# Kernel tuning notes

Hardware: AMD Instinct MI355X
Metric: run time of the kernel (lower is better)

The kernel has to match this reference:

```python
import jax, jax.numpy as jnp
import numpy as np

D_MODEL = 1024
NUM_HEADS = 16
DEPTH = D_MODEL // NUM_HEADS


def setup_inputs() -> dict:
    key = jax.random.key(0)
    ks = jax.random.split(key, 5)
    B, S = 2, 2048
    scale = 1.0 / np.sqrt(D_MODEL)
    x = jax.random.normal(ks[0], (B, S, D_MODEL), dtype=jnp.float32)
    wq = jax.random.normal(ks[1], (D_MODEL, D_MODEL), dtype=jnp.float32) * scale
    wk = jax.random.normal(ks[2], (D_MODEL, D_MODEL), dtype=jnp.float32) * scale
    wv = jax.random.normal(ks[3], (D_MODEL, D_MODEL), dtype=jnp.float32) * scale
    wo = jax.random.normal(ks[4], (D_MODEL, D_MODEL), dtype=jnp.float32) * scale
    zb = jnp.zeros((D_MODEL,), dtype=jnp.float32)
    return {"x": x, "wq": wq, "bq": zb, "wk": wk, "bk": zb, "wv": wv, "bv": zb, "wo": wo, "bo": zb}


def _split_heads(t):
    # [B, S, D] -> [B, H, S, depth]
    B, S, _ = t.shape
    return t.reshape(B, S, NUM_HEADS, DEPTH).transpose(0, 2, 1, 3)


def reference(x, wq, bq, wk, bk, wv, bv, wo, bo):
    q = _split_heads(x @ wq + bq)
    k = _split_heads(x @ wk + bk)
    v = _split_heads(x @ wv + bv)
    scores = jnp.einsum("bhqd,bhkd->bhqk", q, k) / jnp.sqrt(jnp.float32(DEPTH))
    attn = jax.nn.softmax(scores, axis=-1)
    out = jnp.einsum("bhqk,bhkd->bhqd", attn, v)  # [B, H, S, depth]
    B, H, S, d = out.shape
    out = out.transpose(0, 2, 1, 3).reshape(B, S, D_MODEL)
    return out @ wo + bo
```

## Files before the change

### kernel.cpp

```cpp
#include <hip/hip_runtime.h>
#include <stdint.h>

#define SS 2048
#define DM 1024
#define HD 16
#define DP 64
#define BB 2

#define QSCALE 0.18033688011112042f

typedef unsigned short u16;
typedef short bf16x8 __attribute__((ext_vector_type(8)));
typedef float f32x4 __attribute__((ext_vector_type(4)));

#if __has_builtin(__builtin_amdgcn_exp2f)
#define EXP2F __builtin_amdgcn_exp2f
#else
#define EXP2F exp2f
#endif

__device__ __forceinline__ u16 f2b(float f) {
  unsigned u = __builtin_bit_cast(unsigned, f);
  u = (u + 0x7fffu + ((u >> 16) & 1u)) >> 16;
  return (u16)u;
}

__device__ __forceinline__ void gl_lds16(const void* g, void* l) {
  __builtin_amdgcn_global_load_lds(
      (const __attribute__((address_space(1))) unsigned int*)g,
      (__attribute__((address_space(3))) unsigned int*)l, 16, 0, 0);
}

__global__ __launch_bounds__(256) void cast_bf16_kernel(const float* __restrict__ in,
                                                        u16* __restrict__ out, int n) {
  int i = (blockIdx.x * 256 + threadIdx.x) * 4;
  if (i + 3 < n) {
    float4 f = *reinterpret_cast<const float4*>(in + i);
    ushort4 o;
    o.x = f2b(f.x); o.y = f2b(f.y); o.z = f2b(f.z); o.w = f2b(f.w);
    *reinterpret_cast<ushort4*>(out + i) = o;
  }
}

__global__ __launch_bounds__(256) void tcast4_kernel(
    const float* __restrict__ w0, const float* __restrict__ w1,
    const float* __restrict__ w2, const float* __restrict__ w3,
    u16* __restrict__ o0, u16* __restrict__ o1, u16* __restrict__ o2, u16* __restrict__ o3) {
  __shared__ float tile[32][33];
  const int z = blockIdx.z;
  const float* in = z == 0 ? w0 : (z == 1 ? w1 : (z == 2 ? w2 : w3));
  u16* out = z == 0 ? o0 : (z == 1 ? o1 : (z == 2 ? o2 : o3));
  const float scale = z == 0 ? QSCALE : 1.f;
  int tx = threadIdx.x & 31, ty = threadIdx.x >> 5;
  int c0 = blockIdx.x * 32;
  int r0 = blockIdx.y * 32;
#pragma unroll
  for (int j = 0; j < 4; ++j)
    tile[ty + j * 8][tx] = in[(size_t)(r0 + ty + j * 8) * DM + c0 + tx];
  __syncthreads();
#pragma unroll
  for (int j = 0; j < 4; ++j)
    out[(size_t)(c0 + ty + j * 8) * DM + r0 + tx] = f2b(tile[tx][ty + j * 8] * scale);
}

__global__ __launch_bounds__(256) void gemm_qkv(
    const u16* __restrict__ A, const u16* __restrict__ BT,
    const float* __restrict__ b0, const float* __restrict__ b1, const float* __restrict__ b2,
    u16* __restrict__ Oq, u16* __restrict__ Ok, u16* __restrict__ Ovt, int M, int K) {
  __shared__ __align__(16) u16 As[128][32];
  __shared__ __align__(16) u16 Bs[128][32];
  const int t = threadIdx.x;
  const int w = t >> 6, l = t & 63;
  const int lr = l & 15, lg = l >> 4;
  const int wr = w >> 1, wc = w & 1;
  const int m0 = blockIdx.y * 128, n0 = blockIdx.x * 128;

  const u16* Ab = A + (size_t)m0 * K;
  const u16* Bb = BT + (size_t)n0 * K;
  const int arow = t >> 2, achk = (t & 3) * 8;

  f32x4 acc[4][4];
#pragma unroll
  for (int mi = 0; mi < 4; ++mi)
#pragma unroll
    for (int ni = 0; ni < 4; ++ni)
      acc[mi][ni] = (f32x4){0.f, 0.f, 0.f, 0.f};

  char* AsB = (char*)(&As[0][0]);
  char* BsB = (char*)(&Bs[0][0]);

  for (int k0 = 0; k0 < K; k0 += 32) {
    gl_lds16(Ab + (size_t)arow * K + k0 + achk, AsB + t * 16);
    gl_lds16(Ab + (size_t)(arow + 64) * K + k0 + achk, AsB + t * 16 + 4096);
    gl_lds16(Bb + (size_t)arow * K + k0 + achk, BsB + t * 16);
    gl_lds16(Bb + (size_t)(arow + 64) * K + k0 + achk, BsB + t * 16 + 4096);
    __syncthreads();
    bf16x8 af[4], bfr[4];
#pragma unroll
    for (int mi = 0; mi < 4; ++mi)
      af[mi] = *(const bf16x8*)&As[wr * 64 + mi * 16 + lr][lg * 8];
#pragma unroll
    for (int ni = 0; ni < 4; ++ni)
      bfr[ni] = *(const bf16x8*)&Bs[wc * 64 + ni * 16 + lr][lg * 8];
#pragma unroll
    for (int mi = 0; mi < 4; ++mi)
#pragma unroll
      for (int ni = 0; ni < 4; ++ni)
        acc[mi][ni] =
            __builtin_amdgcn_mfma_f32_16x16x32_bf16(af[mi], bfr[ni], acc[mi][ni], 0, 0, 0);
    __syncthreads();
  }

  const int proj = n0 >> 10;
  const float* bias = proj == 0 ? b0 : (proj == 1 ? b1 : b2);
  const float bsc = proj == 0 ? QSCALE : 1.f;
  const int nloc0 = n0 & 1023;
  if (proj == 2) {
#pragma unroll
    for (int mi = 0; mi < 4; ++mi)
#pragma unroll
      for (int ni = 0; ni < 4; ++ni) {
        int gm0 = m0 + wr * 64 + mi * 16 + lg * 4;
        int gn = nloc0 + wc * 64 + ni * 16 + lr;
        int s0 = gm0 & (SS - 1), b = gm0 >> 11;
        int h = gn >> 6, d = gn & 63;
        float bv = bias[gn];
        ushort4 pk;
        pk.x = f2b(acc[mi][ni][0] + bv);
        pk.y = f2b(acc[mi][ni][1] + bv);
        pk.z = f2b(acc[mi][ni][2] + bv);
        pk.w = f2b(acc[mi][ni][3] + bv);
        *reinterpret_cast<ushort4*>(Ovt + (((size_t)(b * HD + h)) * DP + d) * SS + s0) = pk;
      }
  } else {
    u16* Op = proj == 0 ? Oq : Ok;
#pragma unroll
    for (int mi = 0; mi < 4; ++mi)
#pragma unroll
      for (int ni = 0; ni < 4; ++ni)
#pragma unroll
        for (int i = 0; i < 4; ++i) {
          int gm = m0 + wr * 64 + mi * 16 + lg * 4 + i;
          int gn = nloc0 + wc * 64 + ni * 16 + lr;
          float vv = acc[mi][ni][i] + bias[gn] * bsc;
          int s = gm & (SS - 1), b = gm >> 11;
          int h = gn >> 6, d = gn & 63;
          Op[(((size_t)(b * HD + h)) * SS + s) * DP + d] = f2b(vv);
        }
  }
}

__global__ __launch_bounds__(256) void gemm_out(
    const u16* __restrict__ A, const u16* __restrict__ BT, const float* __restrict__ b0,
    float* __restrict__ FO, int M, int K) {
  __shared__ __align__(16) u16 As[128][64];
  __shared__ __align__(16) u16 Bs[64][64];
  const int t = threadIdx.x;
  const int w = t >> 6, l = t & 63;
  const int lr = l & 15, lg = l >> 4;
  const int m0 = blockIdx.y * 128, n0 = blockIdx.x * 64;

  const u16* Ab = A + (size_t)m0 * K;
  const u16* Bb = BT + (size_t)n0 * K;
  const int srow = t >> 3;
  const int schk = ((t & 7) ^ (srow & 7)) * 8;

  f32x4 acc[2][4];
#pragma unroll
  for (int mi = 0; mi < 2; ++mi)
#pragma unroll
    for (int ni = 0; ni < 4; ++ni)
      acc[mi][ni] = (f32x4){0.f, 0.f, 0.f, 0.f};

  char* AsB = (char*)(&As[0][0]);
  char* BsB = (char*)(&Bs[0][0]);

  for (int k0 = 0; k0 < K; k0 += 64) {
#pragma unroll
    for (int j = 0; j < 4; ++j)
      gl_lds16(Ab + (size_t)(srow + 32 * j) * K + k0 + schk, AsB + t * 16 + j * 4096);
#pragma unroll
    for (int j = 0; j < 2; ++j)
      gl_lds16(Bb + (size_t)(srow + 32 * j) * K + k0 + schk, BsB + t * 16 + j * 4096);
    __syncthreads();
    bf16x8 af[2][2], bfr[4][2];
#pragma unroll
    for (int mi = 0; mi < 2; ++mi) {
      int r = w * 32 + mi * 16 + lr;
#pragma unroll
      for (int kk = 0; kk < 2; ++kk)
        af[mi][kk] = *(const bf16x8*)&As[r][(((kk * 4 + lg) ^ (r & 7)) * 8)];
    }
#pragma unroll
    for (int ni = 0; ni < 4; ++ni) {
      int r = ni * 16 + lr;
#pragma unroll
      for (int kk = 0; kk < 2; ++kk)
        bfr[ni][kk] = *(const bf16x8*)&Bs[r][(((kk * 4 + lg) ^ (r & 7)) * 8)];
    }
#pragma unroll
    for (int mi = 0; mi < 2; ++mi)
#pragma unroll
      for (int ni = 0; ni < 4; ++ni)
#pragma unroll
        for (int kk = 0; kk < 2; ++kk)
          acc[mi][ni] =
              __builtin_amdgcn_mfma_f32_16x16x32_bf16(af[mi][kk], bfr[ni][kk], acc[mi][ni], 0, 0, 0);
    __syncthreads();
  }

#pragma unroll
  for (int mi = 0; mi < 2; ++mi)
#pragma unroll
    for (int ni = 0; ni < 4; ++ni)
#pragma unroll
      for (int i = 0; i < 4; ++i) {
        int gm = m0 + w * 32 + mi * 16 + lg * 4 + i;
        int gn = n0 + ni * 16 + lr;
        FO[(size_t)gm * DM + gn] = acc[mi][ni][i] + b0[gn];
      }
}

__global__ __launch_bounds__(512) void attn_kernel(const u16* __restrict__ Q,
                                                   const u16* __restrict__ K,
                                                   const u16* __restrict__ VT,
                                                   u16* __restrict__ O) {
  __shared__ __align__(16) u16 Ks[2][64 * 64];
  __shared__ __align__(16) u16 Vs[2][64 * 64];
  __shared__ __align__(16) u16 Ps[8][16][68];
  const int t = threadIdx.x, w = t >> 6, l = t & 63;
  const int lr = l & 15, lg = l >> 4;
  const int bh = blockIdx.y;
  const int q0 = blockIdx.x * 128;
  const u16* Qb = Q + (size_t)bh * SS * DP;
  const u16* Kb = K + (size_t)bh * SS * DP;
  const u16* Vb = VT + (size_t)bh * DP * SS;

  const int qrow = q0 + w * 16 + lr;
  bf16x8 qf[2];
  qf[0] = *(const bf16x8*)(Qb + (size_t)qrow * DP + lg * 8);
  qf[1] = *(const bf16x8*)(Qb + (size_t)qrow * DP + 32 + lg * 8);

  bf16x8 ones8;
#pragma unroll
  for (int j = 0; j < 8; ++j) ones8[j] = (short)0x3f80;

  f32x4 oacc[4];
  f32x4 lac = (f32x4){0.f, 0.f, 0.f, 0.f};
#pragma unroll
  for (int i = 0; i < 4; ++i) oacc[i] = (f32x4){0.f, 0.f, 0.f, 0.f};

  const int srow = t >> 3;
  const int schk = ((t & 7) ^ (srow & 7)) * 8;

  gl_lds16(Kb + (size_t)srow * DP + schk, (char*)Ks[0] + t * 16);
  gl_lds16(Vb + (size_t)srow * SS + 0 + schk, (char*)Vs[0] + t * 16);
  asm volatile("s_waitcnt vmcnt(0)" ::: "memory");
  __syncthreads();

  int cur = 0;
  for (int t0 = 0; t0 < SS; t0 += 64, cur ^= 1) {
    if (t0 + 64 < SS) {
      gl_lds16(Kb + (size_t)(t0 + 64 + srow) * DP + schk, (char*)Ks[cur ^ 1] + t * 16);
      gl_lds16(Vb + (size_t)srow * SS + (t0 + 64) + schk, (char*)Vs[cur ^ 1] + t * 16);
    }
    const u16* Kc = Ks[cur];
    const u16* Vc = Vs[cur];

    f32x4 sc[4];
#pragma unroll
    for (int n = 0; n < 4; ++n) sc[n] = (f32x4){0.f, 0.f, 0.f, 0.f};
#pragma unroll
    for (int n = 0; n < 4; ++n) {
      int r = n * 16 + lr;
#pragma unroll
      for (int kk = 0; kk < 2; ++kk) {
        int chk = ((kk * 4 + lg) ^ (r & 7)) * 8;
        bf16x8 bk8 = *(const bf16x8*)(Kc + r * 64 + chk);
        sc[n] = __builtin_amdgcn_mfma_f32_16x16x32_bf16(qf[kk], bk8, sc[n], 0, 0, 0);
      }
    }

#pragma unroll
    for (int n = 0; n < 4; ++n)
#pragma unroll
      for (int i = 0; i < 4; ++i)
        Ps[w][lg * 4 + i][n * 16 + lr] = f2b(EXP2F(sc[n][i]));
    asm volatile("s_waitcnt lgkmcnt(0)" ::: "memory");
    bf16x8 pf[2];
    pf[0] = *(const bf16x8*)&Ps[w][lr][lg * 8];
    pf[1] = *(const bf16x8*)&Ps[w][lr][32 + lg * 8];

#pragma unroll
    for (int kk = 0; kk < 2; ++kk)
      lac = __builtin_amdgcn_mfma_f32_16x16x32_bf16(pf[kk], ones8, lac, 0, 0, 0);

#pragma unroll
    for (int n = 0; n < 4; ++n) {
      int r = n * 16 + lr;
#pragma unroll
      for (int kk = 0; kk < 2; ++kk) {
        int chk = ((kk * 4 + lg) ^ (r & 7)) * 8;
        bf16x8 bv8 = *(const bf16x8*)(Vc + r * 64 + chk);
        oacc[n] = __builtin_amdgcn_mfma_f32_16x16x32_bf16(pf[kk], bv8, oacc[n], 0, 0, 0);
      }
    }
    asm volatile("s_waitcnt vmcnt(0)" ::: "memory");
    __syncthreads();
  }

  const int b = bh >> 4, h = bh & 15;
  float inv[4];
#pragma unroll
  for (int i = 0; i < 4; ++i) inv[i] = 1.0f / lac[i];
#pragma unroll
  for (int n = 0; n < 4; ++n)
#pragma unroll
    for (int i = 0; i < 4; ++i) {
      int row = q0 + w * 16 + lg * 4 + i;
      int col = h * 64 + n * 16 + lr;
      O[((size_t)(b * SS + row)) * DM + col] = f2b(oacc[n][i] * inv[i]);
    }
}

extern "C" void kernel_launch(void* const* d_in, const int* in_sizes, int n_in,
                              void* d_out, int out_size, void* d_ws, size_t ws_size,
                              hipStream_t stream) {
  const float* x = (const float*)d_in[0];
  const float* wq = (const float*)d_in[1];
  const float* bq = (const float*)d_in[2];
  const float* wk = (const float*)d_in[3];
  const float* bk = (const float*)d_in[4];
  const float* wv = (const float*)d_in[5];
  const float* bv = (const float*)d_in[6];
  const float* wo = (const float*)d_in[7];
  const float* bo = (const float*)d_in[8];
  float* out = (float*)d_out;

  u16* ws = (u16*)d_ws;
  u16* xb = ws;
  u16* wt3 = ws + 4194304;
  u16* wot = ws + 7340032;
  u16* q = ws + 8388608;
  u16* k = ws + 12582912;
  u16* vt = ws + 16777216;
  u16* o = ws;

  cast_bf16_kernel<<<4096, 256, 0, stream>>>(x, xb, 4194304);
  tcast4_kernel<<<dim3(32, 32, 4), 256, 0, stream>>>(wq, wk, wv, wo, wt3, wt3 + 1048576,
                                                     wt3 + 2097152, wot);

  gemm_qkv<<<dim3(24, 32), 256, 0, stream>>>(xb, wt3, bq, bk, bv, q, k, vt, 4096, 1024);
  attn_kernel<<<dim3(16, 32), 512, 0, stream>>>(q, k, vt, o);
  gemm_out<<<dim3(16, 32), 256, 0, stream>>>(o, wot, bo, out, 4096, 1024);
}
```

Before: 215.2 us.

## Keep attention probabilities in registers via transposed MFMA, widen QKV GEMM K-tile

The attention kernel now computes S^T = K·Q^T, so the exp'd scores already sit in the MFMA B-operand layout. They are packed with v_cvt_pk_bf16_f32 and fed straight into the PV and row-sum MFMAs, which removes the per-tile LDS round trip through Ps. K rows are loaded in a permuted order so that this register layout lines up with V. The kernel also moves to 256-thread blocks of 64 queries with an XCD-aware block-to-head remap, so blocks that share K/V data land on the same die. Separately, the QKV GEMM K-step goes from 32 to 64 with an XOR-swizzled LDS layout, halving the barriers per K; the cost is more LDS per block and harder-to-check index permutations.

New measurement: 197.8 us. 1.09x faster.

```diff
diff --git a/kernel.cpp b/kernel.cpp
--- a/kernel.cpp
+++ b/kernel.cpp
@@ -10,8 +10,10 @@
 #define QSCALE 0.18033688011112042f
 
 typedef unsigned short u16;
+typedef unsigned int u32;
 typedef short bf16x8 __attribute__((ext_vector_type(8)));
 typedef float f32x4 __attribute__((ext_vector_type(4)));
+typedef u32 u32x4 __attribute__((ext_vector_type(4)));
 
 #if __has_builtin(__builtin_amdgcn_exp2f)
 #define EXP2F __builtin_amdgcn_exp2f
@@ -23,6 +25,12 @@
   unsigned u = __builtin_bit_cast(unsigned, f);
   u = (u + 0x7fffu + ((u >> 16) & 1u)) >> 16;
   return (u16)u;
+}
+
+__device__ __forceinline__ u32 pk2(float a, float b) {
+  u32 r;
+  asm("v_cvt_pk_bf16_f32 %0, %1, %2" : "=v"(r) : "v"(a), "v"(b));
+  return r;
 }
 
 __device__ __forceinline__ void gl_lds16(const void* g, void* l) {
@@ -67,8 +75,8 @@
     const u16* __restrict__ A, const u16* __restrict__ BT,
     const float* __restrict__ b0, const float* __restrict__ b1, const float* __restrict__ b2,
     u16* __restrict__ Oq, u16* __restrict__ Ok, u16* __restrict__ Ovt, int M, int K) {
-  __shared__ __align__(16) u16 As[128][32];
-  __shared__ __align__(16) u16 Bs[128][32];
+  __shared__ __align__(16) u16 As[128][64];
+  __shared__ __align__(16) u16 Bs[128][64];
   const int t = threadIdx.x;
   const int w = t >> 6, l = t & 63;
   const int lr = l & 15, lg = l >> 4;
@@ -77,7 +85,8 @@
 
   const u16* Ab = A + (size_t)m0 * K;
   const u16* Bb = BT + (size_t)n0 * K;
-  const int arow = t >> 2, achk = (t & 3) * 8;
+  const int srow = t >> 3;
+  const int schk = ((t & 7) ^ (srow & 7)) * 8;
 
   f32x4 acc[4][4];
 #pragma unroll
@@ -89,25 +98,31 @@
   char* AsB = (char*)(&As[0][0]);
   char* BsB = (char*)(&Bs[0][0]);
 
-  for (int k0 = 0; k0 < K; k0 += 32) {
-    gl_lds16(Ab + (size_t)arow * K + k0 + achk, AsB + t * 16);
-    gl_lds16(Ab + (size_t)(arow + 64) * K + k0 + achk, AsB + t * 16 + 4096);
-    gl_lds16(Bb + (size_t)arow * K + k0 + achk, BsB + t * 16);
-    gl_lds16(Bb + (size_t)(arow + 64) * K + k0 + achk, BsB + t * 16 + 4096);
-    __syncthreads();
-    bf16x8 af[4], bfr[4];
-#pragma unroll
-    for (int mi = 0; mi < 4; ++mi)
-      af[mi] = *(const bf16x8*)&As[wr * 64 + mi * 16 + lr][lg * 8];
-#pragma unroll
-    for (int ni = 0; ni < 4; ++ni)
-      bfr[ni] = *(const bf16x8*)&Bs[wc * 64 + ni * 16 + lr][lg * 8];
-#pragma unroll
-    for (int mi = 0; mi < 4; ++mi)
+  for (int k0 = 0; k0 < K; k0 += 64) {
+#pragma unroll
+    for (int j = 0; j < 4; ++j)
+      gl_lds16(Ab + (size_t)(srow + 32 * j) * K + k0 + schk, AsB + t * 16 + j * 4096);
+#pragma unroll
+    for (int j = 0; j < 4; ++j)
+      gl_lds16(Bb + (size_t)(srow + 32 * j) * K + k0 + schk, BsB + t * 16 + j * 4096);
+    __syncthreads();
+#pragma unroll
+    for (int kk = 0; kk < 2; ++kk) {
+      bf16x8 af[4], bfr[4];
+      const int chk = ((kk * 4 + lg) ^ (lr & 7)) * 8;
+#pragma unroll
+      for (int mi = 0; mi < 4; ++mi)
+        af[mi] = *(const bf16x8*)&As[wr * 64 + mi * 16 + lr][chk];
 #pragma unroll
       for (int ni = 0; ni < 4; ++ni)
-        acc[mi][ni] =
-            __builtin_amdgcn_mfma_f32_16x16x32_bf16(af[mi], bfr[ni], acc[mi][ni], 0, 0, 0);
+        bfr[ni] = *(const bf16x8*)&Bs[wc * 64 + ni * 16 + lr][chk];
+#pragma unroll
+      for (int mi = 0; mi < 4; ++mi)
+#pragma unroll
+        for (int ni = 0; ni < 4; ++ni)
+          acc[mi][ni] =
+              __builtin_amdgcn_mfma_f32_16x16x32_bf16(af[mi], bfr[ni], acc[mi][ni], 0, 0, 0);
+    }
     __syncthreads();
   }
 
@@ -221,17 +236,20 @@
       }
 }
 
-__global__ __launch_bounds__(512) void attn_kernel(const u16* __restrict__ Q,
+__global__ __launch_bounds__(256) void attn_kernel(const u16* __restrict__ Q,
                                                    const u16* __restrict__ K,
                                                    const u16* __restrict__ VT,
                                                    u16* __restrict__ O) {
   __shared__ __align__(16) u16 Ks[2][64 * 64];
   __shared__ __align__(16) u16 Vs[2][64 * 64];
-  __shared__ __align__(16) u16 Ps[8][16][68];
   const int t = threadIdx.x, w = t >> 6, l = t & 63;
   const int lr = l & 15, lg = l >> 4;
-  const int bh = blockIdx.y;
-  const int q0 = blockIdx.x * 128;
+
+  const int wg = blockIdx.y * 32 + blockIdx.x;
+  const int xcd = wg & 7, idx = wg >> 3;
+  const int bh = xcd * 4 + (idx >> 5);
+  const int q0 = (idx & 31) * 64;
+
   const u16* Qb = Q + (size_t)bh * SS * DP;
   const u16* Kb = K + (size_t)bh * SS * DP;
   const u16* Vb = VT + (size_t)bh * DP * SS;
@@ -252,75 +270,76 @@
 
   const int srow = t >> 3;
   const int schk = ((t & 7) ^ (srow & 7)) * 8;
-
-  gl_lds16(Kb + (size_t)srow * DP + schk, (char*)Ks[0] + t * 16);
-  gl_lds16(Vb + (size_t)srow * SS + 0 + schk, (char*)Vs[0] + t * 16);
-  asm volatile("s_waitcnt vmcnt(0)" ::: "memory");
+  const int krow = (srow & 3) | ((srow & 12) << 1) | ((srow & 16) >> 2);
+  const int swz = (lr & 7);
+
+  gl_lds16(Kb + (size_t)krow * DP + schk, (char*)Ks[0] + t * 16);
+  gl_lds16(Kb + (size_t)(krow + 32) * DP + schk, (char*)Ks[0] + 4096 + t * 16);
+  gl_lds16(Vb + (size_t)srow * SS + schk, (char*)Vs[0] + t * 16);
+  gl_lds16(Vb + (size_t)(srow + 32) * SS + schk, (char*)Vs[0] + 4096 + t * 16);
   __syncthreads();
 
   int cur = 0;
   for (int t0 = 0; t0 < SS; t0 += 64, cur ^= 1) {
     if (t0 + 64 < SS) {
-      gl_lds16(Kb + (size_t)(t0 + 64 + srow) * DP + schk, (char*)Ks[cur ^ 1] + t * 16);
+      const u16* Kn = Kb + (size_t)(t0 + 64) * DP;
+      gl_lds16(Kn + (size_t)krow * DP + schk, (char*)Ks[cur ^ 1] + t * 16);
+      gl_lds16(Kn + (size_t)(krow + 32) * DP + schk, (char*)Ks[cur ^ 1] + 4096 + t * 16);
       gl_lds16(Vb + (size_t)srow * SS + (t0 + 64) + schk, (char*)Vs[cur ^ 1] + t * 16);
+      gl_lds16(Vb + (size_t)(srow + 32) * SS + (t0 + 64) + schk, (char*)Vs[cur ^ 1] + 4096 + t * 16);
     }
     const u16* Kc = Ks[cur];
     const u16* Vc = Vs[cur];
 
-    f32x4 sc[4];
-#pragma unroll
-    for (int n = 0; n < 4; ++n) sc[n] = (f32x4){0.f, 0.f, 0.f, 0.f};
-#pragma unroll
-    for (int n = 0; n < 4; ++n) {
-      int r = n * 16 + lr;
+    f32x4 st[4];
+#pragma unroll
+    for (int n = 0; n < 4; ++n) st[n] = (f32x4){0.f, 0.f, 0.f, 0.f};
+#pragma unroll
+    for (int n = 0; n < 4; ++n)
 #pragma unroll
       for (int kk = 0; kk < 2; ++kk) {
-        int chk = ((kk * 4 + lg) ^ (r & 7)) * 8;
-        bf16x8 bk8 = *(const bf16x8*)(Kc + r * 64 + chk);
-        sc[n] = __builtin_amdgcn_mfma_f32_16x16x32_bf16(qf[kk], bk8, sc[n], 0, 0, 0);
+        bf16x8 kf = *(const bf16x8*)(Kc + (n * 16 + lr) * 64 + (((kk * 4 + lg) ^ swz) * 8));
+        st[n] = __builtin_amdgcn_mfma_f32_16x16x32_bf16(kf, qf[kk], st[n], 0, 0, 0);
       }
-    }
-
+
+    float e[4][4];
 #pragma unroll
     for (int n = 0; n < 4; ++n)
 #pragma unroll
-      for (int i = 0; i < 4; ++i)
-        Ps[w][lg * 4 + i][n * 16 + lr] = f2b(EXP2F(sc[n][i]));
-    asm volatile("s_waitcnt lgkmcnt(0)" ::: "memory");
-    bf16x8 pf[2];
-    pf[0] = *(const bf16x8*)&Ps[w][lr][lg * 8];
-    pf[1] = *(const bf16x8*)&Ps[w][lr][32 + lg * 8];
-
-#pragma unroll
-    for (int kk = 0; kk < 2; ++kk)
-      lac = __builtin_amdgcn_mfma_f32_16x16x32_bf16(pf[kk], ones8, lac, 0, 0, 0);
-
-#pragma unroll
-    for (int n = 0; n < 4; ++n) {
-      int r = n * 16 + lr;
-#pragma unroll
-      for (int kk = 0; kk < 2; ++kk) {
-        int chk = ((kk * 4 + lg) ^ (r & 7)) * 8;
-        bf16x8 bv8 = *(const bf16x8*)(Vc + r * 64 + chk);
-        oacc[n] = __builtin_amdgcn_mfma_f32_16x16x32_bf16(pf[kk], bv8, oacc[n], 0, 0, 0);
-      }
-    }
-    asm volatile("s_waitcnt vmcnt(0)" ::: "memory");
+      for (int i = 0; i < 4; ++i) e[n][i] = EXP2F(st[n][i]);
+    u32x4 w0, w1;
+    w0[0] = pk2(e[0][0], e[0][1]); w0[1] = pk2(e[0][2], e[0][3]);
+    w0[2] = pk2(e[1][0], e[1][1]); w0[3] = pk2(e[1][2], e[1][3]);
+    w1[0] = pk2(e[2][0], e[2][1]); w1[1] = pk2(e[2][2], e[2][3]);
+    w1[2] = pk2(e[3][0], e[3][1]); w1[3] = pk2(e[3][2], e[3][3]);
+    bf16x8 pf0 = __builtin_bit_cast(bf16x8, w0);
+    bf16x8 pf1 = __builtin_bit_cast(bf16x8, w1);
+
+    lac = __builtin_amdgcn_mfma_f32_16x16x32_bf16(ones8, pf0, lac, 0, 0, 0);
+    lac = __builtin_amdgcn_mfma_f32_16x16x32_bf16(ones8, pf1, lac, 0, 0, 0);
+
+#pragma unroll
+    for (int m = 0; m < 4; ++m) {
+      bf16x8 vf0 = *(const bf16x8*)(Vc + (m * 16 + lr) * 64 + ((lg ^ swz) * 8));
+      oacc[m] = __builtin_amdgcn_mfma_f32_16x16x32_bf16(vf0, pf0, oacc[m], 0, 0, 0);
+      bf16x8 vf1 = *(const bf16x8*)(Vc + (m * 16 + lr) * 64 + (((4 + lg) ^ swz) * 8));
+      oacc[m] = __builtin_amdgcn_mfma_f32_16x16x32_bf16(vf1, pf1, oacc[m], 0, 0, 0);
+    }
     __syncthreads();
   }
 
   const int b = bh >> 4, h = bh & 15;
-  float inv[4];
-#pragma unroll
-  for (int i = 0; i < 4; ++i) inv[i] = 1.0f / lac[i];
-#pragma unroll
-  for (int n = 0; n < 4; ++n)
-#pragma unroll
-    for (int i = 0; i < 4; ++i) {
-      int row = q0 + w * 16 + lg * 4 + i;
-      int col = h * 64 + n * 16 + lr;
-      O[((size_t)(b * SS + row)) * DM + col] = f2b(oacc[n][i] * inv[i]);
-    }
+  const float inv = 1.0f / lac[0];
+  u16* Orow = O + ((size_t)(b * SS + qrow)) * DM + h * 64;
+#pragma unroll
+  for (int m = 0; m < 4; ++m) {
+    ushort4 pk;
+    pk.x = f2b(oacc[m][0] * inv);
+    pk.y = f2b(oacc[m][1] * inv);
+    pk.z = f2b(oacc[m][2] * inv);
+    pk.w = f2b(oacc[m][3] * inv);
+    *reinterpret_cast<ushort4*>(Orow + m * 16 + lg * 4) = pk;
+  }
 }
 
 extern "C" void kernel_launch(void* const* d_in, const int* in_sizes, int n_in,
@@ -351,6 +370,6 @@
                                                      wt3 + 2097152, wot);
 
   gemm_qkv<<<dim3(24, 32), 256, 0, stream>>>(xb, wt3, bq, bk, bv, q, k, vt, 4096, 1024);
-  attn_kernel<<<dim3(16, 32), 512, 0, stream>>>(q, k, vt, o);
+  attn_kernel<<<dim3(32, 32), 256, 0, stream>>>(q, k, vt, o);
   gemm_out<<<dim3(16, 32), 256, 0, stream>>>(o, wot, bo, out, 4096, 1024);
 }
```
